# Kernel tuning notes

Hardware: AMD Instinct MI355X
Metric: run time of the kernel (lower is better)

## Reference

```python
import jax
jax.config.update("jax_enable_x64", True)
import jax.numpy as jnp
import numpy as np

INPUT_DIM = 2048
NUM_BINS = 32
RMS_EPS = 1e-4  # RunningMeanStd initial count


def setup_inputs() -> dict:
    key = jax.random.key(0)
    k1, k2 = jax.random.split(key)
    features = jax.random.normal(k1, (64, 256, INPUT_DIM), dtype=jnp.float32)
    # register_buffer: randn(input_dim, num_bins) / sqrt(input_dim)
    random_projection = jax.random.normal(k2, (INPUT_DIM, NUM_BINS), dtype=jnp.float32) / np.sqrt(INPUT_DIM)
    return {"features": features, "random_projection": random_projection}


def _occurrence_counts(keys):
    """For each element, 1 + number of earlier elements with the same key.
    Stable argsort keeps original order inside each duplicate run, so the
    rank within a run equals the sequential visit count."""
    n = keys.shape[0]
    order = jnp.argsort(keys)  # stable
    sk = keys[order]
    idx = jnp.arange(n, dtype=jnp.int64)
    new_run = jnp.concatenate([jnp.ones((1,), bool), sk[1:] != sk[:-1]])
    starts = jax.lax.cummax(jnp.where(new_run, idx, 0))
    counts_sorted = idx - starts + 1
    return jnp.zeros(n, jnp.int64).at[order].set(counts_sorted)


def reference(features, random_projection):
    batch, seq, feat = features.shape
    x = features.reshape(-1, feat)
    n = x.shape[0]

    # RunningMeanStd.update from fresh state (mean=0, var=1, count=1e-4)
    bm = jnp.mean(x, axis=0)
    bv = jnp.var(x, axis=0, ddof=1)  # torch .var(dim=0) is unbiased
    tot = RMS_EPS + n
    mean = bm * (n / tot)  # delta = bm - 0
    m2 = 1.0 * RMS_EPS + bv * n + (bm ** 2) * (RMS_EPS * n / tot)
    var = m2 / tot
    sigma = jnp.sqrt(var + 1e-8)

    normalized = (x - mean) / sigma
    projected = normalized @ random_projection  # [n, num_bins]
    bits = (projected > 0).astype(jnp.int64)
    powers = (2 ** jnp.arange(min(NUM_BINS, 63), dtype=jnp.int64))
    h = (bits[:, : powers.shape[0]] * powers).sum(axis=-1)  # < 2^32

    env = jnp.arange(n, dtype=jnp.int64) % batch  # default env_indices path
    keys = h * batch + env  # unique per (env, hash), fits int64
    counts = _occurrence_counts(keys)

    rewards = 1.0 / jnp.sqrt(counts.astype(features.dtype))
    return rewards.reshape(batch, seq, 1)
```

## Files before the change

kernel.cpp:

```cpp
#include <hip/hip_runtime.h>
#include <math.h>

#define FEAT 2048
#define NBINS 32
#define NROWS 16384
#define NCLS 64
#define SB 1024
#define RPB 16

typedef __attribute__((ext_vector_type(8))) short short8;
typedef __attribute__((ext_vector_type(4))) float f32x4;

static __device__ __forceinline__ unsigned int pk2bf(float a, float b) {
    unsigned ua = __float_as_uint(a);
    unsigned ub = __float_as_uint(b);
    ua = (ua + 0x7FFFu + ((ua >> 16) & 1u)) >> 16;
    ub = (ub + 0x7FFFu + ((ub >> 16) & 1u)) & 0xFFFF0000u;
    return ua | ub;
}

__global__ __launch_bounds__(256) void k1_stats(const float* __restrict__ x,
                                                float* __restrict__ pS1,
                                                float* __restrict__ pS2) {
    const int b = blockIdx.x, t = threadIdx.x;
    const float4* xb = reinterpret_cast<const float4*>(x) + (size_t)b * RPB * (FEAT / 4);
    float4 s1a = make_float4(0.f,0.f,0.f,0.f), s1b = make_float4(0.f,0.f,0.f,0.f);
    float4 s2a = make_float4(0.f,0.f,0.f,0.f), s2b = make_float4(0.f,0.f,0.f,0.f);
    #pragma unroll
    for (int r = 0; r < RPB; ++r) {
        const float4 va = xb[(size_t)r * (FEAT / 4) + t];
        const float4 vb = xb[(size_t)r * (FEAT / 4) + t + 256];
        s1a.x += va.x; s1a.y += va.y; s1a.z += va.z; s1a.w += va.w;
        s2a.x += va.x * va.x; s2a.y += va.y * va.y; s2a.z += va.z * va.z; s2a.w += va.w * va.w;
        s1b.x += vb.x; s1b.y += vb.y; s1b.z += vb.z; s1b.w += vb.w;
        s2b.x += vb.x * vb.x; s2b.y += vb.y * vb.y; s2b.z += vb.z * vb.z; s2b.w += vb.w * vb.w;
    }
    float4* o1 = reinterpret_cast<float4*>(pS1 + (size_t)b * FEAT);
    float4* o2 = reinterpret_cast<float4*>(pS2 + (size_t)b * FEAT);
    o1[t] = s1a; o1[t + 256] = s1b;
    o2[t] = s2a; o2[t + 256] = s2b;
}

__global__ __launch_bounds__(256) void k2_final(const float* __restrict__ pS1,
                                                const float* __restrict__ pS2,
                                                const float* __restrict__ P,
                                                float* __restrict__ ms,
                                                unsigned int* __restrict__ QTf) {
    __shared__ double sh1[8][32];
    __shared__ double sh2[8][32];
    __shared__ float isig_sh[32];
    const int t = threadIdx.x;
    const int ci = t & 31, seg = t >> 5;
    const int c = blockIdx.x * 32 + ci;
    const int segN = SB >> 3;
    double S1 = 0.0, S2 = 0.0;
    for (int i = 0; i < segN; ++i) {
        const int k = seg * segN + i;
        S1 += (double)pS1[(size_t)k * FEAT + c];
        S2 += (double)pS2[(size_t)k * FEAT + c];
    }
    sh1[seg][ci] = S1; sh2[seg][ci] = S2;
    __syncthreads();
    if (t < 32) {
        double s1 = 0.0, s2 = 0.0;
        #pragma unroll
        for (int s = 0; s < 8; ++s) { s1 += sh1[s][t]; s2 += sh2[s][t]; }
        const int cc = blockIdx.x * 32 + t;
        const double n = (double)NROWS;
        const double bm = s1 / n;
        const double bv = (s2 - s1 * s1 / n) / (n - 1.0);
        const double tot = 1e-4 + n;
        const double mean = bm * (n / tot);
        const double m2 = 1e-4 + bv * n + bm * bm * (1e-4 * n / tot);
        const double var = m2 / tot;
        const double isig = 1.0 / sqrt(var + 1e-8);
        ms[cc] = (float)(mean * isig);
        isig_sh[t] = (float)isig;
    }
    __syncthreads();
    const int nb = t >> 7;
    const int lane = (t & 127) >> 1;
    const int half = t & 1;
    const int lrow = lane & 15, lk = lane >> 4;
    const int bin = nb * 16 + lrow;
    const int ccl = lk * 8 + half * 4;
    const int cc = blockIdx.x * 32 + ccl;
    unsigned int w0 = pk2bf(P[(size_t)cc * NBINS + bin] * isig_sh[ccl],
                            P[(size_t)(cc + 1) * NBINS + bin] * isig_sh[ccl + 1]);
    unsigned int w1 = pk2bf(P[(size_t)(cc + 2) * NBINS + bin] * isig_sh[ccl + 2],
                            P[(size_t)(cc + 3) * NBINS + bin] * isig_sh[ccl + 3]);
    const int ch = blockIdx.x >> 2, ks = blockIdx.x & 3;
    char* dst = reinterpret_cast<char*>(QTf) +
                (size_t)(((nb * 16 + ch) * 4 + ks) * 1024 + lane * 16 + half * 8);
    uint2 pk; pk.x = w0; pk.y = w1;
    *reinterpret_cast<uint2*>(dst) = pk;
}

__global__ __launch_bounds__(256) void k2b_offset(const float* __restrict__ ms,
                                                  const float* __restrict__ P,
                                                  float* __restrict__ offs) {
    __shared__ double sh[256];
    const int b = blockIdx.x, t = threadIdx.x;
    double s = 0.0;
    for (int f = t; f < FEAT; f += 256) s += (double)ms[f] * (double)P[(size_t)f * NBINS + b];
    sh[t] = s;
    __syncthreads();
    for (int st = 128; st > 0; st >>= 1) {
        if (t < st) sh[t] += sh[t + st];
        __syncthreads();
    }
    if (t == 0) offs[b] = (float)sh[0];
}

__global__ __launch_bounds__(256) void k3_mfma(const float* __restrict__ x,
                                               const unsigned int* __restrict__ QTf,
                                               const float* __restrict__ offs,
                                               unsigned int* __restrict__ hout) {
    const int t = threadIdx.x;
    const int w = t >> 6, l = t & 63;
    const int lrow = l & 15, lk = l >> 4;
    const int bid = blockIdx.x;

    const float* ax = x + (size_t)(bid * 64 + w * 16 + lrow) * FEAT + lk * 8;
    const short8* b0p = reinterpret_cast<const short8*>(QTf) + l;
    const short8* b1p = b0p + 4096;

    f32x4 acc0 = {0.f, 0.f, 0.f, 0.f};
    f32x4 acc1 = {0.f, 0.f, 0.f, 0.f};

    #pragma unroll 8
    for (int ss = 0; ss < 64; ++ss) {
        const float4 va = *reinterpret_cast<const float4*>(ax + ss * 32);
        const float4 vb = *reinterpret_cast<const float4*>(ax + ss * 32 + 4);
        uint4 ap;
        ap.x = pk2bf(va.x, va.y); ap.y = pk2bf(va.z, va.w);
        ap.z = pk2bf(vb.x, vb.y); ap.w = pk2bf(vb.z, vb.w);
        const short8 a  = __builtin_bit_cast(short8, ap);
        const short8 b0 = b0p[ss * 64];
        const short8 b1 = b1p[ss * 64];
        acc0 = __builtin_amdgcn_mfma_f32_16x16x32_bf16(a, b0, acc0, 0, 0, 0);
        acc1 = __builtin_amdgcn_mfma_f32_16x16x32_bf16(a, b1, acc1, 0, 0, 0);
    }

    const float o0 = offs[lrow];
    const float o1 = offs[16 + lrow];
    #pragma unroll
    for (int r = 0; r < 4; ++r) {
        const unsigned long long m0 = __ballot(acc0[r] > o0);
        const unsigned long long m1 = __ballot(acc1[r] > o1);
        if (lrow == 0) {
            const unsigned int h =
                (unsigned int)((m0 >> (16 * lk)) & 0xFFFFull) |
                ((unsigned int)((m1 >> (16 * lk)) & 0xFFFFull) << 16);
            const int irow = w * 16 + lk * 4 + r;
            hout[(size_t)irow * 256 + bid] = h;
        }
    }
}

__global__ __launch_bounds__(256) void k4_count(const unsigned int* __restrict__ hcls,
                                                float* __restrict__ out) {
    __shared__ unsigned int hh[256];
    const int c = blockIdx.x, t = threadIdx.x;
    hh[t] = hcls[(size_t)c * 256 + t];
    __syncthreads();
    const unsigned int mine = hh[t];
    int cnt = 1;
    for (int j = 0; j < 256; ++j) {
        cnt += (j < t && hh[j] == mine) ? 1 : 0;
    }
    out[(size_t)t * NCLS + c] = 1.0f / sqrtf((float)cnt);
}

extern "C" void kernel_launch(void* const* d_in, const int* in_sizes, int n_in,
                              void* d_out, int out_size, void* d_ws, size_t ws_size,
                              hipStream_t stream) {
    const float* x = (const float*)d_in[0];
    const float* P = (const float*)d_in[1];
    float* out = (float*)d_out;
    char* ws = (char*)d_ws;

    float* pS1 = (float*)(ws);
    float* pS2 = (float*)(ws + (size_t)SB * FEAT * 4);
    float* ms  = (float*)(ws + (size_t)16 * 1024 * 1024);
    float* offsB = ms + FEAT;
    unsigned int* QTf = (unsigned int*)(ws + (size_t)17 * 1024 * 1024);
    unsigned int* h   = (unsigned int*)(ws + (size_t)18 * 1024 * 1024);

    k1_stats<<<SB, 256, 0, stream>>>(x, pS1, pS2);
    k2_final<<<64, 256, 0, stream>>>(pS1, pS2, P, ms, QTf);
    k2b_offset<<<32, 256, 0, stream>>>(ms, P, offsB);
    k3_mfma<<<256, 256, 0, stream>>>(x, QTf, offsB, h);
    k4_count<<<NCLS, 256, 0, stream>>>(h, out);
}
```

Baseline: 74.93 us.

## Widen stats reduction grid and split MFMA K dimension across extra waves

The column-statistics finalisation moves to its own kernel over 256 blocks of 8 columns each, replacing 64 blocks of 32. The bf16 fragment packing becomes a separate kernel that reads the inverse sigma from global memory. The projection kernel now uses 512 threads, splitting the K range in half across two wave groups and combining the partial accumulators through shared memory before the sign ballot. The aim is more parallelism and latency hiding in the under-occupied reduction and GEMV stages, at the cost of an extra kernel launch and a block-level sync.

```diff
diff --git a/kernel.cpp b/kernel.cpp
--- a/kernel.cpp
+++ b/kernel.cpp
@@ -41,31 +41,29 @@
     o2[t] = s2a; o2[t + 256] = s2b;
 }
 
-__global__ __launch_bounds__(256) void k2_final(const float* __restrict__ pS1,
+__global__ __launch_bounds__(256) void k2_stats(const float* __restrict__ pS1,
                                                 const float* __restrict__ pS2,
-                                                const float* __restrict__ P,
                                                 float* __restrict__ ms,
-                                                unsigned int* __restrict__ QTf) {
-    __shared__ double sh1[8][32];
-    __shared__ double sh2[8][32];
-    __shared__ float isig_sh[32];
+                                                float* __restrict__ isig_g) {
+    __shared__ double sh1[32][8];
+    __shared__ double sh2[32][8];
     const int t = threadIdx.x;
-    const int ci = t & 31, seg = t >> 5;
-    const int c = blockIdx.x * 32 + ci;
-    const int segN = SB >> 3;
+    const int ci = t & 7, s = t >> 3;
+    const int c = blockIdx.x * 8 + ci;
     double S1 = 0.0, S2 = 0.0;
-    for (int i = 0; i < segN; ++i) {
-        const int k = seg * segN + i;
+    #pragma unroll 4
+    for (int j = 0; j < 32; ++j) {
+        const int k = s * 32 + j;
         S1 += (double)pS1[(size_t)k * FEAT + c];
         S2 += (double)pS2[(size_t)k * FEAT + c];
     }
-    sh1[seg][ci] = S1; sh2[seg][ci] = S2;
-    __syncthreads();
-    if (t < 32) {
+    sh1[s][ci] = S1; sh2[s][ci] = S2;
+    __syncthreads();
+    if (t < 8) {
         double s1 = 0.0, s2 = 0.0;
         #pragma unroll
-        for (int s = 0; s < 8; ++s) { s1 += sh1[s][t]; s2 += sh2[s][t]; }
-        const int cc = blockIdx.x * 32 + t;
+        for (int q = 0; q < 32; ++q) { s1 += sh1[q][t]; s2 += sh2[q][t]; }
+        const int cc = blockIdx.x * 8 + t;
         const double n = (double)NROWS;
         const double bm = s1 / n;
         const double bv = (s2 - s1 * s1 / n) / (n - 1.0);
@@ -75,8 +73,16 @@
         const double var = m2 / tot;
         const double isig = 1.0 / sqrt(var + 1e-8);
         ms[cc] = (float)(mean * isig);
-        isig_sh[t] = (float)isig;
-    }
+        isig_g[cc] = (float)isig;
+    }
+}
+
+__global__ __launch_bounds__(256) void k2q_frag(const float* __restrict__ isig_g,
+                                                const float* __restrict__ P,
+                                                unsigned int* __restrict__ QTf) {
+    __shared__ float isig_sh[32];
+    const int t = threadIdx.x;
+    if (t < 32) isig_sh[t] = isig_g[blockIdx.x * 32 + t];
     __syncthreads();
     const int nb = t >> 7;
     const int lane = (t & 127) >> 1;
@@ -112,24 +118,26 @@
     if (t == 0) offs[b] = (float)sh[0];
 }
 
-__global__ __launch_bounds__(256) void k3_mfma(const float* __restrict__ x,
+__global__ __launch_bounds__(512) void k3_mfma(const float* __restrict__ x,
                                                const unsigned int* __restrict__ QTf,
                                                const float* __restrict__ offs,
                                                unsigned int* __restrict__ hout) {
+    __shared__ f32x4 red[4][2][64];
     const int t = threadIdx.x;
     const int w = t >> 6, l = t & 63;
+    const int rw = w & 3, kh = w >> 2;
     const int lrow = l & 15, lk = l >> 4;
     const int bid = blockIdx.x;
 
-    const float* ax = x + (size_t)(bid * 64 + w * 16 + lrow) * FEAT + lk * 8;
-    const short8* b0p = reinterpret_cast<const short8*>(QTf) + l;
+    const float* ax = x + (size_t)(bid * 64 + rw * 16 + lrow) * FEAT + kh * 1024 + lk * 8;
+    const short8* b0p = reinterpret_cast<const short8*>(QTf) + l + kh * 2048;
     const short8* b1p = b0p + 4096;
 
     f32x4 acc0 = {0.f, 0.f, 0.f, 0.f};
     f32x4 acc1 = {0.f, 0.f, 0.f, 0.f};
 
     #pragma unroll 8
-    for (int ss = 0; ss < 64; ++ss) {
+    for (int ss = 0; ss < 32; ++ss) {
         const float4 va = *reinterpret_cast<const float4*>(ax + ss * 32);
         const float4 vb = *reinterpret_cast<const float4*>(ax + ss * 32 + 4);
         uint4 ap;
@@ -142,18 +150,26 @@
         acc1 = __builtin_amdgcn_mfma_f32_16x16x32_bf16(a, b1, acc1, 0, 0, 0);
     }
 
-    const float o0 = offs[lrow];
-    const float o1 = offs[16 + lrow];
-    #pragma unroll
-    for (int r = 0; r < 4; ++r) {
-        const unsigned long long m0 = __ballot(acc0[r] > o0);
-        const unsigned long long m1 = __ballot(acc1[r] > o1);
-        if (lrow == 0) {
-            const unsigned int h =
-                (unsigned int)((m0 >> (16 * lk)) & 0xFFFFull) |
-                ((unsigned int)((m1 >> (16 * lk)) & 0xFFFFull) << 16);
-            const int irow = w * 16 + lk * 4 + r;
-            hout[(size_t)irow * 256 + bid] = h;
+    if (kh) { red[rw][0][l] = acc0; red[rw][1][l] = acc1; }
+    __syncthreads();
+    if (!kh) {
+        const f32x4 r0 = red[rw][0][l];
+        const f32x4 r1 = red[rw][1][l];
+        acc0 += r0;
+        acc1 += r1;
+        const float o0 = offs[lrow];
+        const float o1 = offs[16 + lrow];
+        #pragma unroll
+        for (int r = 0; r < 4; ++r) {
+            const unsigned long long m0 = __ballot(acc0[r] > o0);
+            const unsigned long long m1 = __ballot(acc1[r] > o1);
+            if (lrow == 0) {
+                const unsigned int h =
+                    (unsigned int)((m0 >> (16 * lk)) & 0xFFFFull) |
+                    ((unsigned int)((m1 >> (16 * lk)) & 0xFFFFull) << 16);
+                const int irow = rw * 16 + lk * 4 + r;
+                hout[(size_t)irow * 256 + bid] = h;
+            }
         }
     }
 }
@@ -183,13 +199,15 @@
     float* pS1 = (float*)(ws);
     float* pS2 = (float*)(ws + (size_t)SB * FEAT * 4);
     float* ms  = (float*)(ws + (size_t)16 * 1024 * 1024);
-    float* offsB = ms + FEAT;
+    float* isig = ms + FEAT;
+    float* offsB = isig + FEAT;
     unsigned int* QTf = (unsigned int*)(ws + (size_t)17 * 1024 * 1024);
     unsigned int* h   = (unsigned int*)(ws + (size_t)18 * 1024 * 1024);
 
     k1_stats<<<SB, 256, 0, stream>>>(x, pS1, pS2);
-    k2_final<<<64, 256, 0, stream>>>(pS1, pS2, P, ms, QTf);
+    k2_stats<<<256, 256, 0, stream>>>(pS1, pS2, ms, isig);
+    k2q_frag<<<64, 256, 0, stream>>>(isig, P, QTf);
     k2b_offset<<<32, 256, 0, stream>>>(ms, P, offsB);
-    k3_mfma<<<256, 256, 0, stream>>>(x, QTf, offsB, h);
+    k3_mfma<<<256, 512, 0, stream>>>(x, QTf, offsB, h);
     k4_count<<<NCLS, 256, 0, stream>>>(h, out);
 }
```

Result: slower. 78.20 us (+4.4%).
